# Optimization experiments

Hardware: AMD Instinct MI355X
Metric: run time of the kernel (lower is better)

The kernel has to match this reference:

```python
import jax, jax.numpy as jnp
import numpy as np

N_TREES = 100
N_TRAIN = 40000
N_QUERY = 1024
N_LEAVES = 512
EPS = 1e-8


def setup_inputs() -> dict:
    key = jax.random.key(0)
    k1, k2 = jax.random.split(key)
    # Per-tree leaf id of each query point: equivalent of tree.apply(X) per tree.
    query_leaf_ids = jax.random.randint(k1, (N_TREES, N_QUERY), 0, N_LEAVES, dtype=jnp.int32)
    # Per-tree leaf id of each training point: equivalent of tree.apply(X_train).
    train_leaf_ids = jax.random.randint(k2, (N_TREES, N_TRAIN), 0, N_LEAVES, dtype=jnp.int32)
    # Uniform vote weight per tree (original sums unit counts then divides by T).
    tree_weights = jnp.ones((N_TREES,), dtype=jnp.float32)
    return {
        "tree_weights": tree_weights,
        "query_leaf_ids": query_leaf_ids,
        "train_leaf_ids": train_leaf_ids,
    }


def reference(tree_weights, query_leaf_ids, train_leaf_ids):
    # weights[m, j] = (1/T) * sum_t tw[t] * 1[leaf_t(query m) == leaf_t(train j)]
    T = tree_weights.shape[0]
    M = query_leaf_ids.shape[1]
    n_train = train_leaf_ids.shape[1]

    def step(acc, inputs):
        tw, q_leaf, tr_leaf = inputs  # scalar, [M], [n_train]
        # Co-membership indicator for this tree: [M, n_train]
        ind = (q_leaf[:, None] == tr_leaf[None, :]).astype(acc.dtype)
        return acc + tw * ind, None

    init = jnp.zeros((M, n_train), dtype=jnp.float32)
    weights, _ = jax.lax.scan(step, init, (tree_weights, query_leaf_ids, train_leaf_ids))
    weights = weights / T  # average over trees
    # Row-normalize so each query's weights sum to 1 (with eps, as in original).
    weights = weights / (jnp.sum(weights, axis=1, keepdims=True) + EPS)
    return weights
```

## Files before the change

kernel.cpp:

```cpp
#include <hip/hip_runtime.h>
#include <hip/hip_bf16.h>
#include <stdint.h>

#define N_TREES  100
#define N_TRAIN  40000
#define N_QUERY  1024
#define N_LEAVES 512
#define N_BINS   1024
#define HALF_J   (N_TRAIN / 2)
#define HALF_W   (HALF_J / 4)
#define PADTRAIN 47168

#define BIDX_BYTES ((size_t)N_TREES * PADTRAIN * 2)
#define BPK_OFF    BIDX_BYTES
#define BPK_BYTES  ((size_t)N_TREES * N_BINS * 4)
#define WS_NEEDED  (BPK_OFF + BPK_BYTES)

__global__ __launch_bounds__(1024) void build(const int* __restrict__ train,
                                              uint32_t* __restrict__ bpk,
                                              uint16_t* __restrict__ bidx) {
    const int t   = blockIdx.x;
    const int tid = threadIdx.x;
    __shared__ __align__(16) uint16_t sorted[PADTRAIN];
    __shared__ uint32_t hist[N_BINS];
    __shared__ uint32_t sbuf[2][N_BINS];
    __shared__ uint32_t cursor[N_BINS];
    __shared__ uint32_t totpad_sh;

    hist[tid] = 0;
    __syncthreads();

    const int4* tr4 = (const int4*)(train + t * N_TRAIN);
    for (int i = tid; i < N_TRAIN / 4; i += 1024) {
        int4 v = tr4[i];
        const int hb = (i * 4 >= HALF_J) ? N_LEAVES : 0;
        atomicAdd(&hist[v.x + hb], 1u);
        atomicAdd(&hist[v.y + hb], 1u);
        atomicAdd(&hist[v.z + hb], 1u);
        atomicAdd(&hist[v.w + hb], 1u);
    }
    __syncthreads();

    const uint32_t len = hist[tid];
    const uint32_t lp  = (len + 7u) & ~7u;
    sbuf[0][tid] = lp;
    __syncthreads();
    int src = 0;
    for (int d = 1; d < N_BINS; d <<= 1) {
        uint32_t v = sbuf[src][tid];
        if (tid >= d) v += sbuf[src][tid - d];
        sbuf[src ^ 1][tid] = v;
        __syncthreads();
        src ^= 1;
    }
    {
        const uint32_t start = sbuf[src][tid] - lp;
        bpk[t * N_BINS + tid] = (len << 16) | start;
        cursor[tid] = start;
        if (tid == N_BINS - 1) totpad_sh = sbuf[src][N_BINS - 1];
    }
    __syncthreads();

    for (int i = tid; i < N_TRAIN / 4; i += 1024) {
        int4 v = tr4[i];
        const int j  = i * 4;
        const int hb = (j >= HALF_J) ? N_LEAVES : 0;
        uint32_t p0 = atomicAdd(&cursor[v.x + hb], 1u); sorted[p0] = (uint16_t)j;
        uint32_t p1 = atomicAdd(&cursor[v.y + hb], 1u); sorted[p1] = (uint16_t)(j + 1);
        uint32_t p2 = atomicAdd(&cursor[v.z + hb], 1u); sorted[p2] = (uint16_t)(j + 2);
        uint32_t p3 = atomicAdd(&cursor[v.w + hb], 1u); sorted[p3] = (uint16_t)(j + 3);
    }
    __syncthreads();

    const uint32_t n16 = (totpad_sh + 7u) >> 3;
    const uint4* s4 = (const uint4*)sorted;
    uint4* g4 = (uint4*)(bidx + (size_t)t * PADTRAIN);
    for (uint32_t i = tid; i < n16; i += 1024) g4[i] = s4[i];
}

__global__ __launch_bounds__(256) void row_kernel(const int* __restrict__ qleaf,
                                                  const uint16_t* __restrict__ bidx,
                                                  const uint32_t* __restrict__ bpk,
                                                  float* __restrict__ out) {
    const int m    = blockIdx.x >> 1;
    const int half = blockIdx.x & 1;
    const int jlo  = half * HALF_J;
    const int tid  = threadIdx.x;
    __shared__ __align__(16) uint32_t cnt[HALF_W];
    __shared__ uint16_t su[N_TREES];
    __shared__ uint16_t lu[N_TREES];
    __shared__ uint16_t luo[N_TREES];
    __shared__ uint16_t cpref[N_TREES + 4];
    __shared__ float    inv_sh;

    uint4* c4 = (uint4*)cnt;
    for (int i = tid; i < HALF_W / 4; i += 256) c4[i] = make_uint4(0, 0, 0, 0);
    if (tid < N_TREES) {
        int q = qleaf[tid * N_QUERY + m];
        uint32_t pk  = bpk[tid * N_BINS + half * N_LEAVES + q];
        uint32_t pko = bpk[tid * N_BINS + (half ^ 1) * N_LEAVES + q];
        su[tid]  = (uint16_t)(pk & 0xffffu);
        lu[tid]  = (uint16_t)(pk >> 16);
        luo[tid] = (uint16_t)(pko >> 16);
    }
    __syncthreads();

    if (tid < 64) {
        int i0 = 2 * tid, i1 = 2 * tid + 1;
        uint32_t l0 = (i0 < N_TREES) ? lu[i0] : 0u;
        uint32_t l1 = (i1 < N_TREES) ? lu[i1] : 0u;
        uint32_t c0 = (l0 + 7u) >> 3, c1 = (l1 + 7u) >> 3;
        uint32_t s   = c0 + c1;
        uint32_t inc = s;
        for (int o = 1; o < 64; o <<= 1) {
            uint32_t v = __shfl_up(inc, o, 64);
            if (tid >= o) inc += v;
        }
        uint32_t excl = inc - s;
        if (i0 < N_TREES) cpref[i0] = (uint16_t)excl;
        if (i1 < N_TREES) cpref[i1] = (uint16_t)(excl + c0);
        if (tid == 63) cpref[N_TREES] = (uint16_t)inc;
        uint32_t tot = l0 + l1;
        tot += ((i0 < N_TREES) ? luo[i0] : 0u) + ((i1 < N_TREES) ? luo[i1] : 0u);
        for (int o = 32; o > 0; o >>= 1) tot += __shfl_down(tot, o, 64);
        if (tid == 0) inv_sh = 1.0f / ((float)tot + 1e-6f);
    }
    __syncthreads();

    const int Ctot = cpref[N_TREES];
    for (int c = tid; c < Ctot; c += 256) {
        int t = 0;
        #pragma unroll
        for (int step = 64; step >= 1; step >>= 1) {
            int cand = t + step;
            if (cand <= N_TREES - 1 && (int)cpref[cand] <= c) t = cand;
        }
        const int cc  = c - (int)cpref[t];
        const int rem = (int)lu[t] - cc * 8;
        const int n   = rem > 8 ? 8 : rem;
        const uint4 w = *(const uint4*)(bidx + (size_t)t * PADTRAIN + su[t] + cc * 8);
        uint32_t e[8] = { w.x & 0xffffu, w.x >> 16, w.y & 0xffffu, w.y >> 16,
                          w.z & 0xffffu, w.z >> 16, w.w & 0xffffu, w.w >> 16 };
        #pragma unroll
        for (int i = 0; i < 8; ++i)
            if (i < n) {
                uint32_t lj = e[i] - (uint32_t)jlo;
                atomicAdd(&cnt[lj >> 2], 1u << ((lj & 3u) * 8u));
            }
    }
    __syncthreads();

    const float inv = inv_sh;
    float4* orow = (float4*)(out + (size_t)m * N_TRAIN + jlo);
    for (int p = tid; p < HALF_W; p += 256) {
        uint32_t w = cnt[p];
        float4 v;
        v.x = (float)(w & 0xffu) * inv;
        v.y = (float)((w >> 8) & 0xffu) * inv;
        v.z = (float)((w >> 16) & 0xffu) * inv;
        v.w = (float)(w >> 24) * inv;
        orow[p] = v;
    }
}

__global__ __launch_bounds__(1024) void row_kernel_direct(const int* __restrict__ qleaf,
                                                          const int* __restrict__ train,
                                                          float* __restrict__ out) {
    const int m   = blockIdx.x;
    const int tid = threadIdx.x;
    __shared__ uint32_t cnt[N_TRAIN / 2];
    __shared__ int      qlds[N_TREES];
    __shared__ uint32_t total_sh;

    if (tid < N_TREES) qlds[tid] = qleaf[tid * N_QUERY + m];
    if (tid == 0) total_sh = 0;
    __syncthreads();

    const int2* tr2 = (const int2*)train;
    for (int p = tid; p < N_TRAIN / 2; p += 1024) {
        uint32_t c0 = 0, c1 = 0;
        for (int t = 0; t < N_TREES; ++t) {
            const int q = qlds[t];
            int2 v = tr2[t * (N_TRAIN / 2) + p];
            c0 += (v.x == q);
            c1 += (v.y == q);
        }
        cnt[p] = c0 | (c1 << 16);
    }
    __syncthreads();

    uint32_t local = 0;
    for (int p = tid; p < N_TRAIN / 2; p += 1024) {
        uint32_t w = cnt[p];
        local += (w & 0xffffu) + (w >> 16);
    }
    const int lane = tid & 63;
    for (int o = 32; o > 0; o >>= 1) local += __shfl_down(local, o, 64);
    if (lane == 0) atomicAdd(&total_sh, local);
    __syncthreads();

    const float inv = 1.0f / ((float)total_sh + 1e-6f);
    float2* orow = (float2*)(out + (size_t)m * N_TRAIN);
    for (int p = tid; p < N_TRAIN / 2; p += 1024) {
        uint32_t w = cnt[p];
        float2 v;
        v.x = (float)(w & 0xffffu) * inv;
        v.y = (float)(w >> 16) * inv;
        orow[p] = v;
    }
}

extern "C" void kernel_launch(void* const* d_in, const int* in_sizes, int n_in,
                              void* d_out, int out_size, void* d_ws, size_t ws_size,
                              hipStream_t stream) {
    const int* qleaf = (const int*)d_in[1];
    const int* train = (const int*)d_in[2];
    float* out = (float*)d_out;

    if (ws_size >= WS_NEEDED) {
        uint16_t* bidx = (uint16_t*)d_ws;
        uint32_t* bpk  = (uint32_t*)((char*)d_ws + BPK_OFF);
        build<<<N_TREES, 1024, 0, stream>>>(train, bpk, bidx);
        row_kernel<<<N_QUERY * 2, 256, 0, stream>>>(qleaf, bidx, bpk, out);
    } else {
        row_kernel_direct<<<N_QUERY, 1024, 0, stream>>>(qleaf, train, out);
    }
}
```

Measured before the change: 52.62 us.

## Split per-tree histogram into separate multi-block kernel before scan/scatter

```diff
diff --git a/kernel.cpp b/kernel.cpp
--- a/kernel.cpp
+++ b/kernel.cpp
@@ -9,39 +9,54 @@
 #define N_BINS   1024
 #define HALF_J   (N_TRAIN / 2)
 #define HALF_W   (HALF_J / 4)
+#define QUART_J  (N_TRAIN / 4)
 #define PADTRAIN 47168
 
 #define BIDX_BYTES ((size_t)N_TREES * PADTRAIN * 2)
 #define BPK_OFF    BIDX_BYTES
 #define BPK_BYTES  ((size_t)N_TREES * N_BINS * 4)
-#define WS_NEEDED  (BPK_OFF + BPK_BYTES)
-
-__global__ __launch_bounds__(1024) void build(const int* __restrict__ train,
-                                              uint32_t* __restrict__ bpk,
-                                              uint16_t* __restrict__ bidx) {
+#define HP_OFF     (BPK_OFF + BPK_BYTES)
+#define HP_BYTES   ((size_t)N_TREES * 4 * N_LEAVES * 4)
+#define WS_NEEDED  (HP_OFF + HP_BYTES)
+
+__global__ __launch_bounds__(256) void hist_part(const int* __restrict__ train,
+                                                 uint32_t* __restrict__ histp) {
+    const int t    = blockIdx.x >> 2;
+    const int part = blockIdx.x & 3;
+    const int tid  = threadIdx.x;
+    __shared__ uint32_t hist[N_LEAVES];
+    for (int i = tid; i < N_LEAVES; i += 256) hist[i] = 0;
+    __syncthreads();
+
+    const int4* tr4 = (const int4*)(train + t * N_TRAIN + part * QUART_J);
+    for (int i = tid; i < QUART_J / 4; i += 256) {
+        int4 v = tr4[i];
+        atomicAdd(&hist[v.x], 1u);
+        atomicAdd(&hist[v.y], 1u);
+        atomicAdd(&hist[v.z], 1u);
+        atomicAdd(&hist[v.w], 1u);
+    }
+    __syncthreads();
+
+    uint32_t* hp = histp + (size_t)(t * 4 + part) * N_LEAVES;
+    for (int i = tid; i < N_LEAVES; i += 256) hp[i] = hist[i];
+}
+
+__global__ __launch_bounds__(1024) void scan_scatter(const int* __restrict__ train,
+                                                     const uint32_t* __restrict__ histp,
+                                                     uint32_t* __restrict__ bpk,
+                                                     uint16_t* __restrict__ bidx) {
     const int t   = blockIdx.x;
     const int tid = threadIdx.x;
     __shared__ __align__(16) uint16_t sorted[PADTRAIN];
-    __shared__ uint32_t hist[N_BINS];
     __shared__ uint32_t sbuf[2][N_BINS];
     __shared__ uint32_t cursor[N_BINS];
     __shared__ uint32_t totpad_sh;
 
-    hist[tid] = 0;
-    __syncthreads();
-
-    const int4* tr4 = (const int4*)(train + t * N_TRAIN);
-    for (int i = tid; i < N_TRAIN / 4; i += 1024) {
-        int4 v = tr4[i];
-        const int hb = (i * 4 >= HALF_J) ? N_LEAVES : 0;
-        atomicAdd(&hist[v.x + hb], 1u);
-        atomicAdd(&hist[v.y + hb], 1u);
-        atomicAdd(&hist[v.z + hb], 1u);
-        atomicAdd(&hist[v.w + hb], 1u);
-    }
-    __syncthreads();
-
-    const uint32_t len = hist[tid];
+    const uint32_t* hp = histp + (size_t)t * 4 * N_LEAVES;
+    const int leaf = tid & (N_LEAVES - 1);
+    const int hoff = (tid >= N_LEAVES) ? 2 * N_LEAVES : 0;
+    const uint32_t len = hp[hoff + leaf] + hp[hoff + N_LEAVES + leaf];
     const uint32_t lp  = (len + 7u) & ~7u;
     sbuf[0][tid] = lp;
     __syncthreads();
@@ -61,6 +76,7 @@
     }
     __syncthreads();
 
+    const int4* tr4 = (const int4*)(train + t * N_TRAIN);
     for (int i = tid; i < N_TRAIN / 4; i += 1024) {
         int4 v = tr4[i];
         const int j  = i * 4;
@@ -218,9 +234,11 @@
     float* out = (float*)d_out;
 
     if (ws_size >= WS_NEEDED) {
-        uint16_t* bidx = (uint16_t*)d_ws;
-        uint32_t* bpk  = (uint32_t*)((char*)d_ws + BPK_OFF);
-        build<<<N_TREES, 1024, 0, stream>>>(train, bpk, bidx);
+        uint16_t* bidx  = (uint16_t*)d_ws;
+        uint32_t* bpk   = (uint32_t*)((char*)d_ws + BPK_OFF);
+        uint32_t* histp = (uint32_t*)((char*)d_ws + HP_OFF);
+        hist_part<<<N_TREES * 4, 256, 0, stream>>>(train, histp);
+        scan_scatter<<<N_TREES, 1024, 0, stream>>>(train, histp, bpk, bidx);
         row_kernel<<<N_QUERY * 2, 256, 0, stream>>>(qleaf, bidx, bpk, out);
     } else {
         row_kernel_direct<<<N_QUERY, 1024, 0, stream>>>(qleaf, train, out);
```

After: 52.66 us. About the same (+0.1%).
